# Kernel optimization log

Hardware: AMD Instinct MI355X
Metric: run time of the kernel (lower is better)

## Reference

```python
import jax, jax.numpy as jnp
import numpy as np
import math

NUM_EMBED = 1024
EMBED_DIM = 256
COMMITMENT_COST = 0.25


def setup_inputs() -> dict:
    key = jax.random.key(0)
    k1, k2 = jax.random.split(key)
    inputs = jax.random.normal(k1, (16, EMBED_DIM, 4096), dtype=jnp.float32)
    embed = jax.random.normal(k2, (NUM_EMBED, EMBED_DIM), dtype=jnp.float32)
    return {"inputs": inputs, "embed": embed}


def reference(inputs, embed):
    sg = jax.lax.stop_gradient
    num_embed = embed.shape[0]
    # channels-first (B, D, T) -> (B, T, D)
    x = jnp.swapaxes(inputs, 1, -1)
    B, T, D = x.shape
    flat = x.reshape(-1, D)  # (N, D)
    # pairwise squared distances to the codebook: (N, K)
    d2 = (jnp.sum(flat * flat, axis=1, keepdims=True)
          + jnp.sum(embed * embed, axis=1)
          - 2.0 * flat @ embed.T)
    q_idx = jnp.argmin(d2, axis=1)  # (N,) int
    # one-hot @ embed is just a gather of the nearest codewords
    z_q = embed[q_idx].reshape(x.shape)  # (B, T, D)
    vq_loss = jnp.mean((z_q - sg(x)) ** 2)
    commitment_loss = jnp.mean((sg(z_q) - x) ** 2)
    loss = vq_loss + COMMITMENT_COST * commitment_loss
    # straight-through estimator
    z_q_st = x + sg(z_q - x)
    # codebook usage stats: probs = mean of the one-hot rows
    n = flat.shape[0]
    probs = jnp.zeros((num_embed,), dtype=flat.dtype).at[q_idx].add(1.0) / n
    perplexity = jnp.exp(-jnp.sum(probs * jnp.log(probs + 1e-10)))
    num_spatial_positions = n / B  # == T
    kldiv_r = (math.log(num_embed) * num_spatial_positions
               * jnp.ones((B, 1), dtype=x.dtype))
    z_q_out = jnp.swapaxes(z_q_st, 1, -1)  # back to (B, D, T)
    return z_q_out, loss, kldiv_r, perplexity
```

## Files before the change

kernel.cpp:

```cpp
#include <hip/hip_runtime.h>
#include <math.h>

#define T_DIM 4096
#define D_DIM 256
#define K_NUM 1024
#define B_NUM 16
#define N_TOT (B_NUM * T_DIM)
#define EPS_FLAG 0.25f

typedef float f32x4 __attribute__((ext_vector_type(4)));
typedef _Float16 half8 __attribute__((ext_vector_type(8)));

#define WS_FLAGCNT 0
#define WS_LOSS 4
#define WS_HIST 64
#define WS_E2 4352
#define WS_QIDX 8704
#define WS_FLAGLIST 270848
#define WS_BESTD 532992
#define WS_ESWZ 795136
#define WS_XROWS 1319424

__device__ inline void gl_lds16(const void* g, void* l) {
    __builtin_amdgcn_global_load_lds(
        (const __attribute__((address_space(1))) unsigned int*)g,
        (__attribute__((address_space(3))) unsigned int*)l, 16, 0, 0);
}

__global__ __launch_bounds__(256) void e2_kernel(const float* __restrict__ embed,
                                                 float* __restrict__ e2) {
    const int wave = threadIdx.x >> 6;
    const int lane = threadIdx.x & 63;
    const int k = blockIdx.x * 4 + wave;
    const float4* row = (const float4*)(embed + (size_t)k * D_DIM);
    float4 v = row[lane];
    float s = v.x * v.x + v.y * v.y + v.z * v.z + v.w * v.w;
    #pragma unroll
    for (int off = 32; off; off >>= 1) s += __shfl_down(s, off);
    if (lane == 0) e2[k] = s;
}

__global__ __launch_bounds__(256) void prep_eswz_kernel(const float* __restrict__ embed,
                                                        unsigned char* __restrict__ eswz) {
    const int tau = blockIdx.x * 256 + threadIdx.x;
    const int g = tau >> 9;
    const int k = (tau >> 6) & 7;
    const int l = tau & 63;
    const int col = g * 16 + (l & 15);
    const int d0 = k * 32 + ((l >> 4) << 3);
    const float* src = embed + (size_t)col * D_DIM + d0;
    half8 h;
    #pragma unroll
    for (int j = 0; j < 8; ++j) h[j] = (_Float16)src[j];
    *(half8*)(eswz + (size_t)g * 8192 + k * 1024 + l * 16) = h;
}

__global__ __launch_bounds__(256, 2) void argmin_mfma_kernel(
    const float* __restrict__ x, const unsigned char* __restrict__ eswz,
    const float* __restrict__ e2, const float* __restrict__ embed,
    int* __restrict__ qidx, int* __restrict__ flagcnt, int* __restrict__ flaglist,
    float* __restrict__ bestd, float* __restrict__ xrows,
    float* __restrict__ out, int* __restrict__ hist,
    float* __restrict__ loss_sum, int cap)
{
    __shared__ __align__(16) unsigned char bbuf[2][16384];
    __shared__ float e2s[K_NUM];
    __shared__ int   qid_lds[128];
    __shared__ int   lrows[128];
    __shared__ float lbest[128];
    __shared__ int   lcnt;
    __shared__ int   gbase;

    const int tid = threadIdx.x;
    const int w = tid >> 6;
    const int l = tid & 63;
    const int rb = blockIdx.x * 128;
    const int b = rb >> 12;
    const float* xb = x + (size_t)b * (D_DIM * T_DIM);
    if (tid == 0) lcnt = 0;

    {
        const unsigned char* src = eswz + (size_t)tid * 16;
        #pragma unroll
        for (int r = 0; r < 4; ++r) gl_lds16(src + r * 4096, &bbuf[0][tid * 16 + r * 4096]);
    }
    for (int i = tid; i < K_NUM; i += 256) e2s[i] = e2[i];

    half8 Ah[2][8];
    float x2v[2];
    #pragma unroll
    for (int f = 0; f < 2; ++f) {
        const int row = rb + w * 32 + f * 16 + (l & 15);
        const int t = row & (T_DIM - 1);
        const float* xp = xb + t;
        float s2 = 0.f;
        #pragma unroll
        for (int k = 0; k < 8; ++k) {
            const int d0 = k * 32 + ((l >> 4) << 3);
            half8 h;
            #pragma unroll
            for (int j = 0; j < 8; ++j) {
                float v = xp[(size_t)(d0 + j) * T_DIM];
                h[j] = (_Float16)v;
                s2 = fmaf(v, v, s2);
            }
            Ah[f][k] = h;
        }
        x2v[f] = s2;
    }
    #pragma unroll
    for (int f = 0; f < 2; ++f) {
        x2v[f] += __shfl_xor(x2v[f], 16);
        x2v[f] += __shfl_xor(x2v[f], 32);
    }
    __syncthreads();

    float bestv[8], secv[8];
    int   besti[8];
    #pragma unroll
    for (int s = 0; s < 8; ++s) { bestv[s] = 3.4e38f; secv[s] = 3.4e38f; besti[s] = 0x7FFFFFFF; }

    for (int g = 0; g < 32; ++g) {
        if (g + 1 < 32) {
            const unsigned char* src = eswz + (size_t)(g + 1) * 16384 + (size_t)tid * 16;
            unsigned char* dst = &bbuf[(g + 1) & 1][tid * 16];
            #pragma unroll
            for (int r = 0; r < 4; ++r) gl_lds16(src + r * 4096, dst + r * 4096);
        }
        const unsigned char* bb = bbuf[g & 1];

        f32x4 a00 = {0.f,0.f,0.f,0.f}, a01 = {0.f,0.f,0.f,0.f};
        f32x4 a10 = {0.f,0.f,0.f,0.f}, a11 = {0.f,0.f,0.f,0.f};
        #pragma unroll
        for (int k = 0; k < 8; ++k) {
            half8 b0 = *(const half8*)(bb + k * 1024 + l * 16);
            half8 b1 = *(const half8*)(bb + 8192 + k * 1024 + l * 16);
            a00 = __builtin_amdgcn_mfma_f32_16x16x32_f16(Ah[0][k], b0, a00, 0, 0, 0);
            a10 = __builtin_amdgcn_mfma_f32_16x16x32_f16(Ah[1][k], b0, a10, 0, 0, 0);
            a01 = __builtin_amdgcn_mfma_f32_16x16x32_f16(Ah[0][k], b1, a01, 0, 0, 0);
            a11 = __builtin_amdgcn_mfma_f32_16x16x32_f16(Ah[1][k], b1, a11, 0, 0, 0);
        }

        const int col0 = g * 32 + (l & 15);
        const float e2a = e2s[col0];
        const float e2b = e2s[col0 + 16];
        #pragma unroll
        for (int f = 0; f < 2; ++f) {
            const f32x4 accA = f ? a10 : a00;
            const f32x4 accB = f ? a11 : a01;
            #pragma unroll
            for (int r = 0; r < 4; ++r) {
                const int s = f * 4 + r;
                float sA = fmaf(-2.f, accA[r], e2a);
                float sB = fmaf(-2.f, accB[r], e2b);
                bool swp = sB < sA;
                float lo = swp ? sB : sA;
                float hi = swp ? sA : sB;
                int   li = swp ? col0 + 16 : col0;
                bool upd = lo < bestv[s];
                float mx = upd ? bestv[s] : lo;
                bestv[s] = upd ? lo : bestv[s];
                besti[s] = upd ? li : besti[s];
                secv[s] = fminf(secv[s], fminf(mx, hi));
            }
        }
        __syncthreads();
    }

    float lossw = 0.f;
    #pragma unroll
    for (int slot = 0; slot < 8; ++slot) {
        float bv = bestv[slot], sv = secv[slot];
        int bi = besti[slot];
        #pragma unroll
        for (int d = 1; d < 16; d <<= 1) {
            float ob = __shfl_xor(bv, d);
            int   oi = __shfl_xor(bi, d);
            float os = __shfl_xor(sv, d);
            bool take = (ob < bv) || (ob == bv && oi < bi);
            float loser = take ? bv : ob;
            bv = take ? ob : bv;
            bi = take ? oi : bi;
            sv = fminf(fminf(sv, os), loser);
        }
        const int srcl = ((l >> 4) << 2) + (slot & 3);
        const float x2r = __shfl(x2v[slot >> 2], srcl);
        if ((l & 15) == 0) {
            const int rloc = w * 32 + (slot >> 2) * 16 + (l >> 4) * 4 + (slot & 3);
            qidx[rb + rloc] = bi;
            qid_lds[rloc] = bi;
            atomicAdd(&hist[bi], 1);
            lossw += bv + x2r;
            if (sv - bv < EPS_FLAG) {
                int lp = atomicAdd(&lcnt, 1);
                lrows[lp] = rb + rloc;
                lbest[lp] = bv;
            }
        }
    }
    lossw += __shfl_down(lossw, 16);
    lossw += __shfl_down(lossw, 32);
    if (l == 0) atomicAdd(loss_sum, lossw);

    __syncthreads();
    const int nloc = lcnt;
    if (tid == 0) gbase = nloc ? atomicAdd(flagcnt, nloc) : 0;
    __syncthreads();
    for (int i = w; i < nloc; i += 4) {
        const int row = lrows[i];
        const int p = gbase + i;
        const bool have = (p < cap);
        if (have) {
            const float* xp = xb + (row & (T_DIM - 1));
            float4 vv;
            vv.x = xp[(size_t)(l * 4 + 0) * T_DIM];
            vv.y = xp[(size_t)(l * 4 + 1) * T_DIM];
            vv.z = xp[(size_t)(l * 4 + 2) * T_DIM];
            vv.w = xp[(size_t)(l * 4 + 3) * T_DIM];
            *(float4*)(xrows + (size_t)p * D_DIM + l * 4) = vv;
        }
        if (l == 0) {
            flaglist[p] = have ? row : (row | 0x80000000);
            bestd[p] = lbest[i];
        }
    }

    float* tile = (float*)bbuf;
    const int t0 = rb & (T_DIM - 1);
    float* outb = out + (size_t)b * (D_DIM * T_DIM);
    for (int c = 0; c < 4; ++c) {
        const int d0 = c * 64;
        __syncthreads();
        {
            const int r = tid & 127;
            const int half = tid >> 7;
            const int qi = qid_lds[r];
            const float4* ep = (const float4*)(embed + (size_t)qi * D_DIM + d0 + half * 32);
            #pragma unroll
            for (int i = 0; i < 8; ++i) {
                const float4 ev = ep[i];
                const int dl = half * 32 + i * 4;
                tile[(dl + 0) * 128 + r] = ev.x;
                tile[(dl + 1) * 128 + r] = ev.y;
                tile[(dl + 2) * 128 + r] = ev.z;
                tile[(dl + 3) * 128 + r] = ev.w;
            }
        }
        __syncthreads();
        #pragma unroll 4
        for (int j = 0; j < 32; ++j) {
            const int flat = j * 256 + tid;
            const int dl = flat >> 7;
            const int rr = flat & 127;
            outb[(size_t)(d0 + dl) * T_DIM + t0 + rr] = tile[dl * 128 + rr];
        }
    }
}

__global__ __launch_bounds__(256) void cleanup_kernel(
    const float* __restrict__ x, const float* __restrict__ xrows,
    const float* __restrict__ embed, const float* __restrict__ e2,
    const int* __restrict__ flagcnt, const int* __restrict__ flaglist,
    int* __restrict__ qidx, const float* __restrict__ bestd,
    float* __restrict__ loss_sum, float* __restrict__ out, int* __restrict__ hist)
{
    __shared__ float xr[8][256];
    __shared__ float rvall[8][256];
    __shared__ int   rixall[8][256];
    __shared__ int   rowss[8];
    const int tid = threadIdx.x;
    int cnt = flagcnt[0];
    if (cnt > N_TOT) cnt = N_TOT;
    for (int base = blockIdx.x * 8; base < cnt; base += gridDim.x * 8) {
        const int nr = (cnt - base < 8) ? (cnt - base) : 8;
        __syncthreads();
        if (tid < 8) rowss[tid] = (tid < nr) ? flaglist[base + tid] : 0;
        __syncthreads();
        #pragma unroll
        for (int r = 0; r < 8; ++r) {
            float v = 0.f;
            if (r < nr) {
                const int fe = rowss[r];
                if (fe >= 0) {
                    v = xrows[(size_t)(base + r) * D_DIM + tid];
                } else {
                    const int row = fe & 0x7FFFFFFF;
                    v = x[(size_t)(row >> 12) * (D_DIM * T_DIM) + (size_t)tid * T_DIM
                          + (row & (T_DIM - 1))];
                }
            }
            xr[r][tid] = v;
        }
        __syncthreads();

        float bv[8]; int bix[8];
        #pragma unroll
        for (int r = 0; r < 8; ++r) { bv[r] = 3.4e38f; bix[r] = 0x7FFFFFFF; }
        for (int q = 0; q < 4; ++q) {
            const int c = q * 256 + tid;
            const float4* ep = (const float4*)(embed + (size_t)c * D_DIM);
            float acc[8];
            #pragma unroll
            for (int r = 0; r < 8; ++r) acc[r] = 0.f;
            #pragma unroll 8
            for (int dd = 0; dd < 64; ++dd) {
                const float4 ev = ep[dd];
                #pragma unroll
                for (int r = 0; r < 8; ++r) {
                    const float4 xv = *(const float4*)&xr[r][dd * 4];
                    acc[r] = fmaf(ev.x, xv.x, acc[r]);
                    acc[r] = fmaf(ev.y, xv.y, acc[r]);
                    acc[r] = fmaf(ev.z, xv.z, acc[r]);
                    acc[r] = fmaf(ev.w, xv.w, acc[r]);
                }
            }
            const float ec = e2[c];
            #pragma unroll
            for (int r = 0; r < 8; ++r) {
                const float s = fmaf(-2.f, acc[r], ec);
                if (s < bv[r] || (s == bv[r] && c < bix[r])) { bv[r] = s; bix[r] = c; }
            }
        }
        #pragma unroll
        for (int r = 0; r < 8; ++r) { rvall[r][tid] = bv[r]; rixall[r][tid] = bix[r]; }
        __syncthreads();
        const int w = tid >> 6, ll = tid & 63;
        #pragma unroll
        for (int rr2 = 0; rr2 < 2; ++rr2) {
            const int r = w * 2 + rr2;
            float mv = 3.4e38f; int mi = 0x7FFFFFFF;
            #pragma unroll
            for (int j = 0; j < 4; ++j) {
                const float v = rvall[r][ll + j * 64];
                const int i2 = rixall[r][ll + j * 64];
                if (v < mv || (v == mv && i2 < mi)) { mv = v; mi = i2; }
            }
            #pragma unroll
            for (int d = 1; d < 64; d <<= 1) {
                const float ov = __shfl_xor(mv, d);
                const int   oi = __shfl_xor(mi, d);
                if (ov < mv || (ov == mv && oi < mi)) { mv = ov; mi = oi; }
            }
            if (r < nr) {
                const int row = rowss[r] & 0x7FFFFFFF;
                const int old = qidx[row];
                if (mi != old) {
                    const int b2 = row >> 12, t2 = row & (T_DIM - 1);
                    const float4 ev = *(const float4*)(embed + (size_t)mi * D_DIM + ll * 4);
                    float* op = out + (size_t)b2 * (D_DIM * T_DIM) + t2;
                    op[(size_t)(ll * 4 + 0) * T_DIM] = ev.x;
                    op[(size_t)(ll * 4 + 1) * T_DIM] = ev.y;
                    op[(size_t)(ll * 4 + 2) * T_DIM] = ev.z;
                    op[(size_t)(ll * 4 + 3) * T_DIM] = ev.w;
                    if (ll == 0) {
                        qidx[row] = mi;
                        atomicAdd(&hist[mi], 1);
                        atomicAdd(&hist[old], -1);
                    }
                }
                if (ll == 0) atomicAdd(loss_sum, mv - bestd[base + r]);
            }
        }
    }
}

__global__ __launch_bounds__(256) void finalize_kernel(
    const int* __restrict__ hist, const float* __restrict__ loss_sum,
    float* __restrict__ out)
{
    const int tid = threadIdx.x;
    float acc = 0.f;
    #pragma unroll
    for (int i = tid; i < K_NUM; i += 256) {
        const float p = (float)hist[i] * (1.f / (float)N_TOT);
        acc += p * logf(p + 1e-10f);
    }
    #pragma unroll
    for (int off = 32; off; off >>= 1) acc += __shfl_down(acc, off);
    __shared__ float ls[4];
    if ((tid & 63) == 0) ls[tid >> 6] = acc;
    __syncthreads();
    if (tid == 0) {
        const float H = -(ls[0] + ls[1] + ls[2] + ls[3]);
        const size_t base = (size_t)N_TOT * D_DIM;
        out[base] = 1.25f * loss_sum[0] * (1.f / 16777216.f);
        const float kld = (float)(6.931471805599453 * 4096.0);
        #pragma unroll
        for (int i = 0; i < 16; ++i) out[base + 1 + i] = kld;
        out[base + 17] = expf(H);
    }
}

extern "C" void kernel_launch(void* const* d_in, const int* in_sizes, int n_in,
                              void* d_out, int out_size, void* d_ws, size_t ws_size,
                              hipStream_t stream)
{
    const float* x     = (const float*)d_in[0];
    const float* embed = (const float*)d_in[1];
    float* out = (float*)d_out;

    char* ws = (char*)d_ws;
    int*   flagcnt  = (int*)(ws + WS_FLAGCNT);
    float* loss_sum = (float*)(ws + WS_LOSS);
    int*   hist     = (int*)(ws + WS_HIST);
    float* e2       = (float*)(ws + WS_E2);
    int*   qidx     = (int*)(ws + WS_QIDX);
    int*   flaglist = (int*)(ws + WS_FLAGLIST);
    float* bestd    = (float*)(ws + WS_BESTD);
    unsigned char* eswz = (unsigned char*)(ws + WS_ESWZ);
    float* xrows    = (float*)(ws + WS_XROWS);

    int cap = 0;
    if (ws_size > (size_t)WS_XROWS + 1024) {
        size_t c = (ws_size - WS_XROWS) / 1024;
        cap = (c > (size_t)N_TOT) ? N_TOT : (int)c;
    }

    hipMemsetAsync(ws, 0, 4160, stream);

    e2_kernel<<<K_NUM / 4, 256, 0, stream>>>(embed, e2);
    prep_eswz_kernel<<<128, 256, 0, stream>>>(embed, eswz);
    argmin_mfma_kernel<<<N_TOT / 128, 256, 0, stream>>>(x, eswz, e2, embed, qidx,
                                                        flagcnt, flaglist, bestd, xrows,
                                                        out, hist, loss_sum, cap);
    cleanup_kernel<<<512, 256, 0, stream>>>(x, xrows, embed, e2, flagcnt, flaglist,
                                            qidx, bestd, loss_sum, out, hist);
    finalize_kernel<<<1, 256, 0, stream>>>(hist, loss_sum, out);
}
```

Measured before the change: 288.9 us.

## Register-prefetch codebook tiles, pack argmin into sortable keys, fuse launches

The main loop now loads codebook tiles straight into registers with a double buffer. This removes the global-to-LDS staging and the per-tile __syncthreads. The e2 bias is folded into the MFMA accumulator init, and the best/second candidates are tracked as packed unsigned keys that carry the tile index in the low 6 bits, so the argmin step becomes integer min/max. The prep kernels are merged and also zero the workspace, replacing the memset, and the finalize kernel is folded into the cleanup kernel through a last-block counter. The cost is truncated distance precision in the keys, which the flag/cleanup path has to absorb, plus higher register pressure.

Result: no change. 291.9 us (+1.1%).

```diff
diff --git a/kernel.cpp b/kernel.cpp
--- a/kernel.cpp
+++ b/kernel.cpp
@@ -13,6 +13,7 @@
 
 #define WS_FLAGCNT 0
 #define WS_LOSS 4
+#define WS_DONE 8
 #define WS_HIST 64
 #define WS_E2 4352
 #define WS_QIDX 8704
@@ -21,39 +22,81 @@
 #define WS_ESWZ 795136
 #define WS_XROWS 1319424
 
-__device__ inline void gl_lds16(const void* g, void* l) {
-    __builtin_amdgcn_global_load_lds(
-        (const __attribute__((address_space(1))) unsigned int*)g,
-        (__attribute__((address_space(3))) unsigned int*)l, 16, 0, 0);
+__device__ inline unsigned umin_(unsigned a, unsigned b) { return a < b ? a : b; }
+__device__ inline unsigned umax_(unsigned a, unsigned b) { return a > b ? a : b; }
+
+__global__ __launch_bounds__(256) void prep_kernel(const float* __restrict__ embed,
+                                                   unsigned char* __restrict__ eswz,
+                                                   float* __restrict__ e2,
+                                                   int* __restrict__ wszero) {
+    const int tid = threadIdx.x;
+    if (blockIdx.x == 0) {
+        #pragma unroll
+        for (int i = tid; i < 1040; i += 256) wszero[i] = 0;
+    }
+    const int col = blockIdx.x * 8 + (tid >> 5);
+    const int c = tid & 31;
+    const float* src = embed + (size_t)col * D_DIM + c * 8;
+    half8 h;
+    float s = 0.f;
+    #pragma unroll
+    for (int j = 0; j < 8; ++j) {
+        float v = src[j];
+        h[j] = (_Float16)v;
+        s = fmaf(v, v, s);
+    }
+    const int g = col >> 4;
+    const int k = c >> 2;
+    const int l = ((c & 3) << 4) | (col & 15);
+    *(half8*)(eswz + (size_t)g * 8192 + k * 1024 + l * 16) = h;
+    #pragma unroll
+    for (int off = 16; off; off >>= 1) s += __shfl_down(s, off);
+    if ((tid & 31) == 0) e2[col] = s;
 }
 
-__global__ __launch_bounds__(256) void e2_kernel(const float* __restrict__ embed,
-                                                 float* __restrict__ e2) {
-    const int wave = threadIdx.x >> 6;
-    const int lane = threadIdx.x & 63;
-    const int k = blockIdx.x * 4 + wave;
-    const float4* row = (const float4*)(embed + (size_t)k * D_DIM);
-    float4 v = row[lane];
-    float s = v.x * v.x + v.y * v.y + v.z * v.z + v.w * v.w;
-    #pragma unroll
-    for (int off = 32; off; off >>= 1) s += __shfl_down(s, off);
-    if (lane == 0) e2[k] = s;
-}
-
-__global__ __launch_bounds__(256) void prep_eswz_kernel(const float* __restrict__ embed,
-                                                        unsigned char* __restrict__ eswz) {
-    const int tau = blockIdx.x * 256 + threadIdx.x;
-    const int g = tau >> 9;
-    const int k = (tau >> 6) & 7;
-    const int l = tau & 63;
-    const int col = g * 16 + (l & 15);
-    const int d0 = k * 32 + ((l >> 4) << 3);
-    const float* src = embed + (size_t)col * D_DIM + d0;
-    half8 h;
-    #pragma unroll
-    for (int j = 0; j < 8; ++j) h[j] = (_Float16)src[j];
-    *(half8*)(eswz + (size_t)g * 8192 + k * 1024 + l * 16) = h;
-}
+#define LOADB(BUF, P) do {                                                        \
+    const unsigned char* _bp = eswz + (size_t)(P) * 8192 + (size_t)(l * 16);      \
+    _Pragma("unroll")                                                             \
+    for (int _k = 0; _k < 8; ++_k) BUF[_k] = *(const half8*)(_bp + _k * 1024);    \
+} while (0)
+
+#define PHASE(BUF, P) do {                                                                     \
+    const float _bias = fmaf(e2s[(P) * 16 + (l & 15)], -0.5f, -1024.f);                        \
+    f32x4 c0e = {_bias, _bias, _bias, _bias};                                                  \
+    f32x4 c1e = {_bias, _bias, _bias, _bias};                                                  \
+    f32x4 c0o = {0.f, 0.f, 0.f, 0.f};                                                          \
+    f32x4 c1o = {0.f, 0.f, 0.f, 0.f};                                                          \
+    c0e = __builtin_amdgcn_mfma_f32_16x16x32_f16(Ah[0][0], BUF[0], c0e, 0, 0, 0);              \
+    c1e = __builtin_amdgcn_mfma_f32_16x16x32_f16(Ah[1][0], BUF[0], c1e, 0, 0, 0);              \
+    c0o = __builtin_amdgcn_mfma_f32_16x16x32_f16(Ah[0][1], BUF[1], c0o, 0, 0, 0);              \
+    c1o = __builtin_amdgcn_mfma_f32_16x16x32_f16(Ah[1][1], BUF[1], c1o, 0, 0, 0);              \
+    c0e = __builtin_amdgcn_mfma_f32_16x16x32_f16(Ah[0][2], BUF[2], c0e, 0, 0, 0);              \
+    c1e = __builtin_amdgcn_mfma_f32_16x16x32_f16(Ah[1][2], BUF[2], c1e, 0, 0, 0);              \
+    c0o = __builtin_amdgcn_mfma_f32_16x16x32_f16(Ah[0][3], BUF[3], c0o, 0, 0, 0);              \
+    c1o = __builtin_amdgcn_mfma_f32_16x16x32_f16(Ah[1][3], BUF[3], c1o, 0, 0, 0);              \
+    c0e = __builtin_amdgcn_mfma_f32_16x16x32_f16(Ah[0][4], BUF[4], c0e, 0, 0, 0);              \
+    c1e = __builtin_amdgcn_mfma_f32_16x16x32_f16(Ah[1][4], BUF[4], c1e, 0, 0, 0);              \
+    c0o = __builtin_amdgcn_mfma_f32_16x16x32_f16(Ah[0][5], BUF[5], c0o, 0, 0, 0);              \
+    c1o = __builtin_amdgcn_mfma_f32_16x16x32_f16(Ah[1][5], BUF[5], c1o, 0, 0, 0);              \
+    c0e = __builtin_amdgcn_mfma_f32_16x16x32_f16(Ah[0][6], BUF[6], c0e, 0, 0, 0);              \
+    c1e = __builtin_amdgcn_mfma_f32_16x16x32_f16(Ah[1][6], BUF[6], c1e, 0, 0, 0);              \
+    c0o = __builtin_amdgcn_mfma_f32_16x16x32_f16(Ah[0][7], BUF[7], c0o, 0, 0, 0);              \
+    c1o = __builtin_amdgcn_mfma_f32_16x16x32_f16(Ah[1][7], BUF[7], c1o, 0, 0, 0);              \
+    const unsigned _tag = (unsigned)(P);                                                       \
+    _Pragma("unroll")                                                                          \
+    for (int _r = 0; _r < 4; ++_r) {                                                           \
+        float d0v = (c0e[_r] + c0o[_r]) * -2.f;                                                \
+        float d1v = (c1e[_r] + c1o[_r]) * -2.f;                                                \
+        unsigned k0 = (__float_as_uint(d0v) & 0xFFFFFFC0u) | _tag;                             \
+        unsigned k1 = (__float_as_uint(d1v) & 0xFFFFFFC0u) | _tag;                             \
+        unsigned m0 = umax_(bestk[_r], k0);                                                    \
+        bestk[_r] = umin_(bestk[_r], k0);                                                      \
+        seck[_r] = umin_(seck[_r], m0);                                                        \
+        unsigned m1 = umax_(bestk[4 + _r], k1);                                                \
+        bestk[4 + _r] = umin_(bestk[4 + _r], k1);                                              \
+        seck[4 + _r] = umin_(seck[4 + _r], m1);                                                \
+    }                                                                                          \
+} while (0)
 
 __global__ __launch_bounds__(256, 2) void argmin_mfma_kernel(
     const float* __restrict__ x, const unsigned char* __restrict__ eswz,
@@ -63,8 +106,8 @@
     float* __restrict__ out, int* __restrict__ hist,
     float* __restrict__ loss_sum, int cap)
 {
-    __shared__ __align__(16) unsigned char bbuf[2][16384];
     __shared__ float e2s[K_NUM];
+    __shared__ __align__(16) float tile[64 * 128];
     __shared__ int   qid_lds[128];
     __shared__ int   lrows[128];
     __shared__ float lbest[128];
@@ -79,11 +122,9 @@
     const float* xb = x + (size_t)b * (D_DIM * T_DIM);
     if (tid == 0) lcnt = 0;
 
-    {
-        const unsigned char* src = eswz + (size_t)tid * 16;
-        #pragma unroll
-        for (int r = 0; r < 4; ++r) gl_lds16(src + r * 4096, &bbuf[0][tid * 16 + r * 4096]);
-    }
+    half8 B0[8], B1[8];
+    LOADB(B0, 0);
+
     for (int i = tid; i < K_NUM; i += 256) e2s[i] = e2[i];
 
     half8 Ah[2][8];
@@ -115,63 +156,26 @@
     }
     __syncthreads();
 
-    float bestv[8], secv[8];
-    int   besti[8];
-    #pragma unroll
-    for (int s = 0; s < 8; ++s) { bestv[s] = 3.4e38f; secv[s] = 3.4e38f; besti[s] = 0x7FFFFFFF; }
-
-    for (int g = 0; g < 32; ++g) {
-        if (g + 1 < 32) {
-            const unsigned char* src = eswz + (size_t)(g + 1) * 16384 + (size_t)tid * 16;
-            unsigned char* dst = &bbuf[(g + 1) & 1][tid * 16];
-            #pragma unroll
-            for (int r = 0; r < 4; ++r) gl_lds16(src + r * 4096, dst + r * 4096);
-        }
-        const unsigned char* bb = bbuf[g & 1];
-
-        f32x4 a00 = {0.f,0.f,0.f,0.f}, a01 = {0.f,0.f,0.f,0.f};
-        f32x4 a10 = {0.f,0.f,0.f,0.f}, a11 = {0.f,0.f,0.f,0.f};
-        #pragma unroll
-        for (int k = 0; k < 8; ++k) {
-            half8 b0 = *(const half8*)(bb + k * 1024 + l * 16);
-            half8 b1 = *(const half8*)(bb + 8192 + k * 1024 + l * 16);
-            a00 = __builtin_amdgcn_mfma_f32_16x16x32_f16(Ah[0][k], b0, a00, 0, 0, 0);
-            a10 = __builtin_amdgcn_mfma_f32_16x16x32_f16(Ah[1][k], b0, a10, 0, 0, 0);
-            a01 = __builtin_amdgcn_mfma_f32_16x16x32_f16(Ah[0][k], b1, a01, 0, 0, 0);
-            a11 = __builtin_amdgcn_mfma_f32_16x16x32_f16(Ah[1][k], b1, a11, 0, 0, 0);
-        }
-
-        const int col0 = g * 32 + (l & 15);
-        const float e2a = e2s[col0];
-        const float e2b = e2s[col0 + 16];
-        #pragma unroll
-        for (int f = 0; f < 2; ++f) {
-            const f32x4 accA = f ? a10 : a00;
-            const f32x4 accB = f ? a11 : a01;
-            #pragma unroll
-            for (int r = 0; r < 4; ++r) {
-                const int s = f * 4 + r;
-                float sA = fmaf(-2.f, accA[r], e2a);
-                float sB = fmaf(-2.f, accB[r], e2b);
-                bool swp = sB < sA;
-                float lo = swp ? sB : sA;
-                float hi = swp ? sA : sB;
-                int   li = swp ? col0 + 16 : col0;
-                bool upd = lo < bestv[s];
-                float mx = upd ? bestv[s] : lo;
-                bestv[s] = upd ? lo : bestv[s];
-                besti[s] = upd ? li : besti[s];
-                secv[s] = fminf(secv[s], fminf(mx, hi));
-            }
-        }
-        __syncthreads();
-    }
+    unsigned bestk[8], seck[8];
+    #pragma unroll
+    for (int s = 0; s < 8; ++s) { bestk[s] = 0xFFFFFFFFu; seck[s] = 0xFFFFFFFFu; }
+
+    for (int pp = 0; pp < 31; ++pp) {
+        LOADB(B1, 2 * pp + 1);
+        PHASE(B0, 2 * pp);
+        LOADB(B0, 2 * pp + 2);
+        PHASE(B1, 2 * pp + 1);
+    }
+    LOADB(B1, 63);
+    PHASE(B0, 62);
+    PHASE(B1, 63);
 
     float lossw = 0.f;
     #pragma unroll
     for (int slot = 0; slot < 8; ++slot) {
-        float bv = bestv[slot], sv = secv[slot];
-        int bi = besti[slot];
+        float bv = __uint_as_float(bestk[slot] & 0xFFFFFFC0u) - 2048.f;
+        float sv = __uint_as_float(seck[slot] & 0xFFFFFFC0u) - 2048.f;
+        int bi = (int)(bestk[slot] & 63u) * 16 + (l & 15);
         #pragma unroll
         for (int d = 1; d < 16; d <<= 1) {
             float ob = __shfl_xor(bv, d);
@@ -225,7 +229,6 @@
         }
     }
 
-    float* tile = (float*)bbuf;
     const int t0 = rb & (T_DIM - 1);
     float* outb = out + (size_t)b * (D_DIM * T_DIM);
     for (int c = 0; c < 4; ++c) {
@@ -262,12 +265,14 @@
     const float* __restrict__ embed, const float* __restrict__ e2,
     const int* __restrict__ flagcnt, const int* __restrict__ flaglist,
     int* __restrict__ qidx, const float* __restrict__ bestd,
-    float* __restrict__ loss_sum, float* __restrict__ out, int* __restrict__ hist)
+    float* __restrict__ loss_sum, float* __restrict__ out, int* __restrict__ hist,
+    int* __restrict__ donecnt)
 {
     __shared__ float xr[8][256];
     __shared__ float rvall[8][256];
     __shared__ int   rixall[8][256];
     __shared__ int   rowss[8];
+    __shared__ int   amlast;
     const int tid = threadIdx.x;
     int cnt = flagcnt[0];
     if (cnt > N_TOT) cnt = N_TOT;
@@ -362,32 +367,37 @@
             }
         }
     }
-}
-
-__global__ __launch_bounds__(256) void finalize_kernel(
-    const int* __restrict__ hist, const float* __restrict__ loss_sum,
-    float* __restrict__ out)
-{
-    const int tid = threadIdx.x;
-    float acc = 0.f;
-    #pragma unroll
-    for (int i = tid; i < K_NUM; i += 256) {
-        const float p = (float)hist[i] * (1.f / (float)N_TOT);
-        acc += p * logf(p + 1e-10f);
-    }
-    #pragma unroll
-    for (int off = 32; off; off >>= 1) acc += __shfl_down(acc, off);
-    __shared__ float ls[4];
-    if ((tid & 63) == 0) ls[tid >> 6] = acc;
+
+    __threadfence();
+    if (tid == 0) {
+        const int old = atomicAdd(donecnt, 1);
+        amlast = (old == (int)gridDim.x - 1) ? 1 : 0;
+    }
     __syncthreads();
-    if (tid == 0) {
-        const float H = -(ls[0] + ls[1] + ls[2] + ls[3]);
-        const size_t base = (size_t)N_TOT * D_DIM;
-        out[base] = 1.25f * loss_sum[0] * (1.f / 16777216.f);
-        const float kld = (float)(6.931471805599453 * 4096.0);
-        #pragma unroll
-        for (int i = 0; i < 16; ++i) out[base + 1 + i] = kld;
-        out[base + 17] = expf(H);
+    if (amlast) {
+        float acc = 0.f;
+        for (int i = tid; i < K_NUM; i += 256) {
+            const int h = __hip_atomic_load(&hist[i], __ATOMIC_RELAXED,
+                                            __HIP_MEMORY_SCOPE_AGENT);
+            const float p = (float)h * (1.f / (float)N_TOT);
+            acc += p * logf(p + 1e-10f);
+        }
+        #pragma unroll
+        for (int off = 32; off; off >>= 1) acc += __shfl_down(acc, off);
+        __shared__ float ls[4];
+        if ((tid & 63) == 0) ls[tid >> 6] = acc;
+        __syncthreads();
+        if (tid == 0) {
+            const float H = -(ls[0] + ls[1] + ls[2] + ls[3]);
+            const float L = __hip_atomic_load(loss_sum, __ATOMIC_RELAXED,
+                                              __HIP_MEMORY_SCOPE_AGENT);
+            const size_t base = (size_t)N_TOT * D_DIM;
+            out[base] = 1.25f * L * (1.f / 16777216.f);
+            const float kld = (float)(6.931471805599453 * 4096.0);
+            #pragma unroll
+            for (int i = 0; i < 16; ++i) out[base + 1 + i] = kld;
+            out[base + 17] = expf(H);
+        }
     }
 }
 
@@ -402,6 +412,7 @@
     char* ws = (char*)d_ws;
     int*   flagcnt  = (int*)(ws + WS_FLAGCNT);
     float* loss_sum = (float*)(ws + WS_LOSS);
+    int*   donecnt  = (int*)(ws + WS_DONE);
     int*   hist     = (int*)(ws + WS_HIST);
     float* e2       = (float*)(ws + WS_E2);
     int*   qidx     = (int*)(ws + WS_QIDX);
@@ -416,14 +427,10 @@
         cap = (c > (size_t)N_TOT) ? N_TOT : (int)c;
     }
 
-    hipMemsetAsync(ws, 0, 4160, stream);
-
-    e2_kernel<<<K_NUM / 4, 256, 0, stream>>>(embed, e2);
-    prep_eswz_kernel<<<128, 256, 0, stream>>>(embed, eswz);
+    prep_kernel<<<128, 256, 0, stream>>>(embed, eswz, e2, (int*)ws);
     argmin_mfma_kernel<<<N_TOT / 128, 256, 0, stream>>>(x, eswz, e2, embed, qidx,
                                                         flagcnt, flaglist, bestd, xrows,
                                                         out, hist, loss_sum, cap);
-    cleanup_kernel<<<512, 256, 0, stream>>>(x, xrows, embed, e2, flagcnt, flaglist,
-                                            qidx, bestd, loss_sum, out, hist);
-    finalize_kernel<<<1, 256, 0, stream>>>(hist, loss_sum, out);
+    cleanup_kernel<<<256, 256, 0, stream>>>(x, xrows, embed, e2, flagcnt, flaglist,
+                                            qidx, bestd, loss_sum, out, hist, donecnt);
 }
```
